# Kernel tuning notes

Measured on AMD Instinct MI355X. Metric: run time of the kernel, lower is better.

## Reference

```python
import jax, jax.numpy as jnp
import numpy as np

B, N, DIM_S, E = 128, 2048, 128, 128


def _xavier(key, shape):
    fan_out, fan_in = shape[0], shape[1]
    limit = float(np.sqrt(6.0 / (fan_in + fan_out)))
    return jax.random.uniform(key, shape, jnp.float32, -limit, limit)


def setup_inputs() -> dict:
    key = jax.random.key(0)
    ks = jax.random.split(key, 14)
    return {
        "instance": jax.random.normal(ks[0], (B, N, DIM_S), jnp.float32),
        # conv1d kernel-size-1 embeds == per-node linear layers [out, in]
        "W_s": _xavier(ks[1], (E, DIM_S)),
        "b_s": jnp.zeros((E,), jnp.float32),
        "W_a": _xavier(ks[2], (E, E)),
        "b_a": jnp.zeros((E,), jnp.float32),
        "v_a": jax.random.normal(ks[3], (E,), jnp.float32),
        "W_c": _xavier(ks[4], (E, 2 * E)),
        "b_c": jnp.zeros((E,), jnp.float32),
        "v_c": jax.random.normal(ks[5], (E,), jnp.float32),
        "W1": _xavier(ks[6], (E, E)),
        "b1": jnp.zeros((E,), jnp.float32),
        "W2": _xavier(ks[7], (1, E)),
        "b2": jnp.zeros((1,), jnp.float32),
    }


def reference(instance, W_s, b_s, W_a, b_a, v_a, W_c, b_c, v_c, W1, b1, W2, b2):
    # project_s: conv1d k=1 == linear over feature dim. [B,N,E]
    proj = jnp.einsum("bns,es->bne", instance, W_s) + b_s
    # first additive-attention score: v_a . tanh(w_a(proj))  -> [B,N]
    u_t = jnp.einsum("bne,e->bn", jnp.tanh(jnp.einsum("bne,fe->bnf", proj, W_a) + b_a), v_a)
    a_t = jax.nn.softmax(u_t, axis=1)  # softmax over nodes
    c_t = a_t[:, :, None] * proj  # [B,N,E]
    hidden_2 = jnp.concatenate([proj, c_t], axis=2)  # [B,N,2E]
    u_t_2 = jnp.einsum("bne,e->bn", jnp.tanh(jnp.einsum("bnf,ef->bne", hidden_2, W_c) + b_c), v_c)
    prob = jax.nn.softmax(u_t_2, axis=1)  # [B,N]
    h_i = jnp.einsum("bn,bne->be", prob, proj)  # weighted sum -> [B,E]
    out1 = jax.nn.relu(h_i @ W1.T + b1)  # [B,E]
    v = (out1 @ W2.T + b2)[:, 0]  # [B]
    return v
```

## Files before the change

### kernel.cpp

```cpp
#include <hip/hip_runtime.h>
#include <hip/hip_bf16.h>

typedef _Float16 half8 __attribute__((ext_vector_type(8)));
typedef _Float16 half4v __attribute__((ext_vector_type(4)));
typedef float f32x4 __attribute__((ext_vector_type(4)));

#define SWZ(byte, r) ((unsigned)(byte) ^ ((((unsigned)(r)) & 7u) << 4))

constexpr int Bb = 128;
constexpr int Nn = 2048;
constexpr int Ee = 128;
constexpr int BM = 64;
constexpr int NBLK = (Bb * Nn) / BM;

constexpr size_t OFF_W    = 0;
constexpr size_t OFF_PROJ = 131072;
constexpr size_t OFF_UT   = OFF_PROJ + (size_t)Bb * Nn * Ee * 2;
constexpr size_t OFF_AT   = OFF_UT   + (size_t)Bb * Nn * 4;
constexpr size_t OFF_UT2  = OFF_AT   + (size_t)Bb * Nn * 4;
constexpr size_t OFF_PROB = OFF_UT2  + (size_t)Bb * Nn * 4;
constexpr size_t OFF_HP   = OFF_PROB + (size_t)Bb * Nn * 4;

__device__ __forceinline__ void cp16(void* lds, const void* g) {
    __builtin_amdgcn_global_load_lds(
        (const __attribute__((address_space(1))) unsigned int*)g,
        (__attribute__((address_space(3))) unsigned int*)lds, 16, 0, 0);
}

__device__ __forceinline__ float fast_tanh(float x) {
    float e = __expf(2.0f * x);
    return 1.0f - 2.0f * __builtin_amdgcn_rcpf(e + 1.0f);
}

__global__ __launch_bounds__(256) void k_prep(const float* __restrict__ Ws,
                                              const float* __restrict__ Wa,
                                              const float* __restrict__ Wc,
                                              char* __restrict__ wdst)
{
    int id = blockIdx.x * 256 + threadIdx.x;
    for (int i = id; i < 65536; i += 64 * 256) {
        int mat = i >> 14;
        int rem = i & 16383;
        int r = rem >> 7, c = rem & 127;
        float v;
        if      (mat == 0) v = Ws[r * 128 + c];
        else if (mat == 1) v = Wa[r * 128 + c];
        else if (mat == 2) v = Wc[r * 256 + c];
        else               v = Wc[r * 256 + 128 + c];
        unsigned off = SWZ((unsigned)((r * 128 + c) * 2), r);
        *reinterpret_cast<_Float16*>(wdst + (size_t)mat * 32768 + off) = (_Float16)v;
    }
}

__global__ __launch_bounds__(256) void k_pass1(const float* __restrict__ inst,
                                               const char* __restrict__ wtiles,
                                               const float* __restrict__ bs,
                                               const float* __restrict__ ba,
                                               const float* __restrict__ va,
                                               char* __restrict__ projg,
                                               float* __restrict__ ut)
{
    __shared__ _Float16 ldsA[BM * 128];
    __shared__ _Float16 ldsW[128 * 128];

    const int tid  = threadIdx.x;
    const int lane = tid & 63;
    const int w    = tid >> 6;
    const int l15  = lane & 15;
    const int kg   = lane >> 4;
    const size_t row0 = (size_t)blockIdx.x * BM;

    float4 v[8];
    {
        const float* src = inst + row0 * 128;
        #pragma unroll
        for (int i = 0; i < 8; ++i)
            v[i] = *reinterpret_cast<const float4*>(src + (size_t)(i * 256 + tid) * 4);
    }
    #pragma unroll
    for (int i = 0; i < 8; ++i) {
        unsigned o = (unsigned)((i * 256 + tid) * 16);
        cp16((char*)ldsW + o, wtiles + o);
    }
    #pragma unroll
    for (int i = 0; i < 8; ++i) {
        int f = i * 256 + tid;
        int r = f >> 5, c4 = f & 31;
        half4v h = { (_Float16)v[i].x, (_Float16)v[i].y, (_Float16)v[i].z, (_Float16)v[i].w };
        unsigned off = SWZ((unsigned)(r * 256 + c4 * 8), r);
        *reinterpret_cast<half4v*>((char*)ldsA + off) = h;
    }
    __syncthreads();

    const int arow = w * 16 + l15;

    f32x4 acc[8];
    #pragma unroll
    for (int fr = 0; fr < 8; ++fr) acc[fr] = f32x4{0.f, 0.f, 0.f, 0.f};
    #pragma unroll
    for (int kk = 0; kk < 4; ++kk) {
        unsigned aoff = SWZ((unsigned)(arow * 256 + kk * 64 + kg * 16), arow);
        half8 af = *reinterpret_cast<const half8*>((char*)ldsA + aoff);
        #pragma unroll
        for (int fr = 0; fr < 8; ++fr) {
            int br = fr * 16 + l15;
            unsigned boff = SWZ((unsigned)(br * 256 + kk * 64 + kg * 16), br);
            half8 bf = *reinterpret_cast<const half8*>((char*)ldsW + boff);
            acc[fr] = __builtin_amdgcn_mfma_f32_16x16x32_f16(af, bf, acc[fr], 0, 0, 0);
        }
    }
    __syncthreads();

    #pragma unroll
    for (int i = 0; i < 8; ++i) {
        unsigned o = (unsigned)((i * 256 + tid) * 16);
        cp16((char*)ldsW + o, wtiles + 32768 + o);
    }
    #pragma unroll
    for (int fr = 0; fr < 8; ++fr) {
        int e = fr * 16 + l15;
        float bsv = bs[e];
        #pragma unroll
        for (int j = 0; j < 4; ++j) {
            int r = w * 16 + kg * 4 + j;
            float pv = acc[fr][j] + bsv;
            unsigned off = SWZ((unsigned)(r * 256 + e * 2), r);
            *reinterpret_cast<_Float16*>((char*)ldsA + off) = (_Float16)pv;
        }
    }
    __syncthreads();

    {
        char* dst = projg + row0 * 256;
        #pragma unroll
        for (int i = 0; i < 4; ++i) {
            unsigned o = (unsigned)((i * 256 + tid) * 16);
            *reinterpret_cast<uint4*>(dst + o) =
                *reinterpret_cast<const uint4*>((const char*)ldsA + o);
        }
    }

    f32x4 tac[8];
    #pragma unroll
    for (int fr = 0; fr < 8; ++fr) tac[fr] = f32x4{0.f, 0.f, 0.f, 0.f};
    #pragma unroll
    for (int kk = 0; kk < 4; ++kk) {
        unsigned aoff = SWZ((unsigned)(arow * 256 + kk * 64 + kg * 16), arow);
        half8 af = *reinterpret_cast<const half8*>((char*)ldsA + aoff);
        #pragma unroll
        for (int fr = 0; fr < 8; ++fr) {
            int br = fr * 16 + l15;
            unsigned boff = SWZ((unsigned)(br * 256 + kk * 64 + kg * 16), br);
            half8 bf = *reinterpret_cast<const half8*>((char*)ldsW + boff);
            tac[fr] = __builtin_amdgcn_mfma_f32_16x16x32_f16(af, bf, tac[fr], 0, 0, 0);
        }
    }
    float u[4] = {0.f, 0.f, 0.f, 0.f};
    #pragma unroll
    for (int fr = 0; fr < 8; ++fr) {
        int fcol = fr * 16 + l15;
        float vav = va[fcol], bav = ba[fcol];
        #pragma unroll
        for (int j = 0; j < 4; ++j)
            u[j] += vav * fast_tanh(tac[fr][j] + bav);
    }
    #pragma unroll
    for (int d = 1; d < 16; d <<= 1) {
        #pragma unroll
        for (int j = 0; j < 4; ++j) u[j] += __shfl_xor(u[j], d);
    }
    if (l15 == 0) {
        #pragma unroll
        for (int j = 0; j < 4; ++j)
            ut[row0 + w * 16 + kg * 4 + j] = u[j];
    }
}

__global__ __launch_bounds__(256) void k_softmax(const float* __restrict__ x,
                                                 float* __restrict__ y)
{
    __shared__ float red[4];
    const int b = blockIdx.x, tid = threadIdx.x;
    const int lane = tid & 63, w = tid >> 6;
    const float* xb = x + (size_t)b * Nn;
    float4 v0 = *reinterpret_cast<const float4*>(xb + tid * 8);
    float4 v1 = *reinterpret_cast<const float4*>(xb + tid * 8 + 4);
    float m = fmaxf(fmaxf(fmaxf(v0.x, v0.y), fmaxf(v0.z, v0.w)),
                    fmaxf(fmaxf(v1.x, v1.y), fmaxf(v1.z, v1.w)));
    #pragma unroll
    for (int d = 1; d < 64; d <<= 1) m = fmaxf(m, __shfl_xor(m, d));
    if (lane == 0) red[w] = m;
    __syncthreads();
    float M = fmaxf(fmaxf(red[0], red[1]), fmaxf(red[2], red[3]));
    float e[8] = { __expf(v0.x - M), __expf(v0.y - M), __expf(v0.z - M), __expf(v0.w - M),
                   __expf(v1.x - M), __expf(v1.y - M), __expf(v1.z - M), __expf(v1.w - M) };
    float s = 0.f;
    #pragma unroll
    for (int i = 0; i < 8; ++i) s += e[i];
    #pragma unroll
    for (int d = 1; d < 64; d <<= 1) s += __shfl_xor(s, d);
    __syncthreads();
    if (lane == 0) red[w] = s;
    __syncthreads();
    float inv = 1.0f / (red[0] + red[1] + red[2] + red[3]);
    float* yb = y + (size_t)b * Nn;
    float4 o0 = { e[0] * inv, e[1] * inv, e[2] * inv, e[3] * inv };
    float4 o1 = { e[4] * inv, e[5] * inv, e[6] * inv, e[7] * inv };
    *reinterpret_cast<float4*>(yb + tid * 8)     = o0;
    *reinterpret_cast<float4*>(yb + tid * 8 + 4) = o1;
}

__global__ __launch_bounds__(256) void k_pass2(const char* __restrict__ projg,
                                               const char* __restrict__ wtiles,
                                               const float* __restrict__ bc,
                                               const float* __restrict__ vc,
                                               const float* __restrict__ at,
                                               float* __restrict__ ut2)
{
    __shared__ _Float16 ldsP [BM * 128];
    __shared__ _Float16 ldsW1[128 * 128];
    __shared__ _Float16 ldsW2[128 * 128];

    const int tid  = threadIdx.x;
    const int lane = tid & 63;
    const int w    = tid >> 6;
    const int l15  = lane & 15;
    const int kg   = lane >> 4;
    const size_t row0 = (size_t)blockIdx.x * BM;

    {
        const char* src = projg + row0 * 256;
        #pragma unroll
        for (int i = 0; i < 4; ++i) {
            unsigned o = (unsigned)((i * 256 + tid) * 16);
            cp16((char*)ldsP + o, src + o);
        }
    }
    #pragma unroll
    for (int i = 0; i < 8; ++i) {
        unsigned o = (unsigned)((i * 256 + tid) * 16);
        cp16((char*)ldsW1 + o, wtiles + 65536 + o);
    }
    #pragma unroll
    for (int i = 0; i < 8; ++i) {
        unsigned o = (unsigned)((i * 256 + tid) * 16);
        cp16((char*)ldsW2 + o, wtiles + 98304 + o);
    }
    float aj[4];
    #pragma unroll
    for (int j = 0; j < 4; ++j) aj[j] = at[row0 + w * 16 + kg * 4 + j];
    __syncthreads();

    const int arow = w * 16 + l15;
    f32x4 u1[8], u2[8];
    #pragma unroll
    for (int fr = 0; fr < 8; ++fr) { u1[fr] = f32x4{0.f,0.f,0.f,0.f}; u2[fr] = f32x4{0.f,0.f,0.f,0.f}; }
    #pragma unroll
    for (int kk = 0; kk < 4; ++kk) {
        unsigned aoff = SWZ((unsigned)(arow * 256 + kk * 64 + kg * 16), arow);
        half8 af = *reinterpret_cast<const half8*>((char*)ldsP + aoff);
        #pragma unroll
        for (int fr = 0; fr < 8; ++fr) {
            int br = fr * 16 + l15;
            unsigned boff = SWZ((unsigned)(br * 256 + kk * 64 + kg * 16), br);
            half8 bf1 = *reinterpret_cast<const half8*>((char*)ldsW1 + boff);
            u1[fr] = __builtin_amdgcn_mfma_f32_16x16x32_f16(af, bf1, u1[fr], 0, 0, 0);
            half8 bf2 = *reinterpret_cast<const half8*>((char*)ldsW2 + boff);
            u2[fr] = __builtin_amdgcn_mfma_f32_16x16x32_f16(af, bf2, u2[fr], 0, 0, 0);
        }
    }

    float u[4] = {0.f, 0.f, 0.f, 0.f};
    #pragma unroll
    for (int fr = 0; fr < 8; ++fr) {
        int fcol = fr * 16 + l15;
        float vcv = vc[fcol], bcv = bc[fcol];
        #pragma unroll
        for (int j = 0; j < 4; ++j)
            u[j] += vcv * fast_tanh(u1[fr][j] + aj[j] * u2[fr][j] + bcv);
    }
    #pragma unroll
    for (int d = 1; d < 16; d <<= 1) {
        #pragma unroll
        for (int j = 0; j < 4; ++j) u[j] += __shfl_xor(u[j], d);
    }
    if (l15 == 0) {
        #pragma unroll
        for (int j = 0; j < 4; ++j)
            ut2[row0 + w * 16 + kg * 4 + j] = u[j];
    }
}

__global__ __launch_bounds__(256) void k_hi(const float* __restrict__ prob,
                                            const char* __restrict__ projg,
                                            float* __restrict__ hpart)
{
    __shared__ float pw[128];
    __shared__ float hp[16][128];

    const int bid = blockIdx.x;
    const int b = bid >> 4, chunk = bid & 15;
    const int n0 = chunk * 128;
    const int tid = threadIdx.x;
    const int rg = tid >> 4, c16 = tid & 15;

    if (tid < 128) pw[tid] = prob[(size_t)b * Nn + n0 + tid];
    __syncthreads();

    const char* pb = projg + ((size_t)b * Nn + n0) * 256;
    float acc[8] = {0.f,0.f,0.f,0.f,0.f,0.f,0.f,0.f};
    #pragma unroll
    for (int it = 0; it < 8; ++it) {
        int nl = rg + it * 16;
        float wgt = pw[nl];
        unsigned off = (unsigned)(nl * 256 + ((c16 * 16) ^ ((nl & 7) << 4)));
        half8 ph = *reinterpret_cast<const half8*>(pb + off);
        #pragma unroll
        for (int j = 0; j < 8; ++j) acc[j] += wgt * (float)ph[j];
    }
    #pragma unroll
    for (int j = 0; j < 8; ++j) hp[rg][c16 * 8 + j] = acc[j];
    __syncthreads();
    if (tid < 128) {
        float s = 0.f;
        #pragma unroll
        for (int k = 0; k < 16; ++k) s += hp[k][tid];
        hpart[((size_t)b * 16 + chunk) * 128 + tid] = s;
    }
}

__global__ __launch_bounds__(128) void k_head(const float* __restrict__ hpart,
                                              const float* __restrict__ W1,
                                              const float* __restrict__ b1,
                                              const float* __restrict__ W2,
                                              const float* __restrict__ b2,
                                              float* __restrict__ out)
{
    __shared__ float h[128];
    __shared__ float o1[128];
    const int b = blockIdx.x, tid = threadIdx.x;

    float s = 0.f;
    #pragma unroll
    for (int c = 0; c < 16; ++c) s += hpart[((size_t)b * 16 + c) * 128 + tid];
    h[tid] = s;
    __syncthreads();

    const float* wr = W1 + tid * 128;
    float o = b1[tid];
    #pragma unroll 8
    for (int e = 0; e < 128; e += 4) {
        float4 wv = *reinterpret_cast<const float4*>(wr + e);
        o += wv.x * h[e] + wv.y * h[e+1] + wv.z * h[e+2] + wv.w * h[e+3];
    }
    o1[tid] = fmaxf(o, 0.f);
    __syncthreads();

    if (tid < 64) {
        float p = o1[tid] * W2[tid] + o1[tid + 64] * W2[tid + 64];
        #pragma unroll
        for (int d = 1; d < 64; d <<= 1) p += __shfl_xor(p, d);
        if (tid == 0) out[b] = p + b2[0];
    }
}

extern "C" void kernel_launch(void* const* d_in, const int* in_sizes, int n_in,
                              void* d_out, int out_size, void* d_ws, size_t ws_size,
                              hipStream_t stream)
{
    const float* inst = (const float*)d_in[0];
    const float* Ws   = (const float*)d_in[1];
    const float* bs   = (const float*)d_in[2];
    const float* Wa   = (const float*)d_in[3];
    const float* ba   = (const float*)d_in[4];
    const float* va   = (const float*)d_in[5];
    const float* Wc   = (const float*)d_in[6];
    const float* bc   = (const float*)d_in[7];
    const float* vc   = (const float*)d_in[8];
    const float* W1   = (const float*)d_in[9];
    const float* b1   = (const float*)d_in[10];
    const float* W2   = (const float*)d_in[11];
    const float* b2   = (const float*)d_in[12];
    float* out = (float*)d_out;

    char*  ws     = (char*)d_ws;
    char*  wtiles = ws + OFF_W;
    char*  projg  = ws + OFF_PROJ;
    float* ut     = (float*)(ws + OFF_UT);
    float* at     = (float*)(ws + OFF_AT);
    float* ut2    = (float*)(ws + OFF_UT2);
    float* prob   = (float*)(ws + OFF_PROB);
    float* hpart  = (float*)(ws + OFF_HP);

    hipLaunchKernelGGL(k_prep,    dim3(64),   dim3(256), 0, stream, Ws, Wa, Wc, wtiles);
    hipLaunchKernelGGL(k_pass1,   dim3(NBLK), dim3(256), 0, stream, inst, wtiles, bs, ba, va, projg, ut);
    hipLaunchKernelGGL(k_softmax, dim3(Bb),   dim3(256), 0, stream, ut, at);
    hipLaunchKernelGGL(k_pass2,   dim3(NBLK), dim3(256), 0, stream, projg, wtiles, bc, vc, at, ut2);
    hipLaunchKernelGGL(k_softmax, dim3(Bb),   dim3(256), 0, stream, ut2, prob);
    hipLaunchKernelGGL(k_hi,      dim3(Bb*16),dim3(256), 0, stream, prob, projg, hpart);
    hipLaunchKernelGGL(k_head,    dim3(Bb),   dim3(128), 0, stream, hpart, W1, b1, W2, b2, out);
}
```

Baseline: 284.8 us.

## Make attention passes persistent with double-buffered LDS and fuse softmaxes

```diff
diff --git a/kernel.cpp b/kernel.cpp
--- a/kernel.cpp
+++ b/kernel.cpp
@@ -10,16 +10,15 @@
 constexpr int Bb = 128;
 constexpr int Nn = 2048;
 constexpr int Ee = 128;
-constexpr int BM = 64;
-constexpr int NBLK = (Bb * Nn) / BM;
+constexpr int BM1 = 128;
+constexpr int P1_BLOCKS = 256;
+constexpr int P1_ITERS = (Bb * Nn) / BM1 / P1_BLOCKS;
 
 constexpr size_t OFF_W    = 0;
 constexpr size_t OFF_PROJ = 131072;
 constexpr size_t OFF_UT   = OFF_PROJ + (size_t)Bb * Nn * Ee * 2;
-constexpr size_t OFF_AT   = OFF_UT   + (size_t)Bb * Nn * 4;
-constexpr size_t OFF_UT2  = OFF_AT   + (size_t)Bb * Nn * 4;
-constexpr size_t OFF_PROB = OFF_UT2  + (size_t)Bb * Nn * 4;
-constexpr size_t OFF_HP   = OFF_PROB + (size_t)Bb * Nn * 4;
+constexpr size_t OFF_UT2  = OFF_UT   + (size_t)Bb * Nn * 4;
+constexpr size_t OFF_HP   = OFF_UT2  + (size_t)Bb * Nn * 4;
 
 __device__ __forceinline__ void cp16(void* lds, const void* g) {
     __builtin_amdgcn_global_load_lds(
@@ -52,7 +51,7 @@
     }
 }
 
-__global__ __launch_bounds__(256) void k_pass1(const float* __restrict__ inst,
+__global__ __launch_bounds__(512) void k_pass1(const float* __restrict__ inst,
                                                const char* __restrict__ wtiles,
                                                const float* __restrict__ bs,
                                                const float* __restrict__ ba,
@@ -60,258 +59,301 @@
                                                char* __restrict__ projg,
                                                float* __restrict__ ut)
 {
-    __shared__ _Float16 ldsA[BM * 128];
-    __shared__ _Float16 ldsW[128 * 128];
+    __shared__ _Float16 ldsW[2 * 16384];
+    __shared__ _Float16 bufA[2][16384];
 
     const int tid  = threadIdx.x;
     const int lane = tid & 63;
     const int w    = tid >> 6;
     const int l15  = lane & 15;
     const int kg   = lane >> 4;
-    const size_t row0 = (size_t)blockIdx.x * BM;
-
+    const int arow = w * 16 + l15;
+
+    #pragma unroll
+    for (int i = 0; i < 8; ++i) {
+        unsigned o = (unsigned)((i * 512 + tid) * 16);
+        cp16((char*)ldsW + o, wtiles + o);
+    }
+
+    const size_t tile0 = (size_t)blockIdx.x * P1_ITERS;
     float4 v[8];
     {
-        const float* src = inst + row0 * 128;
+        const float* src = inst + tile0 * BM1 * 128;
         #pragma unroll
         for (int i = 0; i < 8; ++i)
-            v[i] = *reinterpret_cast<const float4*>(src + (size_t)(i * 256 + tid) * 4);
+            v[i] = *reinterpret_cast<const float4*>(src + (size_t)(i * 512 + tid) * 4);
     }
     #pragma unroll
     for (int i = 0; i < 8; ++i) {
-        unsigned o = (unsigned)((i * 256 + tid) * 16);
-        cp16((char*)ldsW + o, wtiles + o);
-    }
-    #pragma unroll
-    for (int i = 0; i < 8; ++i) {
-        int f = i * 256 + tid;
+        int f = i * 512 + tid;
         int r = f >> 5, c4 = f & 31;
         half4v h = { (_Float16)v[i].x, (_Float16)v[i].y, (_Float16)v[i].z, (_Float16)v[i].w };
-        unsigned off = SWZ((unsigned)(r * 256 + c4 * 8), r);
-        *reinterpret_cast<half4v*>((char*)ldsA + off) = h;
-    }
-    __syncthreads();
-
-    const int arow = w * 16 + l15;
-
-    f32x4 acc[8];
-    #pragma unroll
-    for (int fr = 0; fr < 8; ++fr) acc[fr] = f32x4{0.f, 0.f, 0.f, 0.f};
-    #pragma unroll
-    for (int kk = 0; kk < 4; ++kk) {
-        unsigned aoff = SWZ((unsigned)(arow * 256 + kk * 64 + kg * 16), arow);
-        half8 af = *reinterpret_cast<const half8*>((char*)ldsA + aoff);
+        *reinterpret_cast<half4v*>((char*)bufA[0] + SWZ(r * 256 + c4 * 8, r)) = h;
+    }
+    __syncthreads();
+
+    for (int it = 0; it < P1_ITERS; ++it) {
+        const int cur = it & 1, nxt = cur ^ 1;
+        const size_t row0 = (tile0 + it) * BM1;
+
+        if (it + 1 < P1_ITERS) {
+            const float* src = inst + (row0 + BM1) * 128;
+            #pragma unroll
+            for (int i = 0; i < 8; ++i)
+                v[i] = *reinterpret_cast<const float4*>(src + (size_t)(i * 512 + tid) * 4);
+        }
+
+        f32x4 acc[8];
+        #pragma unroll
+        for (int fr = 0; fr < 8; ++fr) acc[fr] = f32x4{0.f, 0.f, 0.f, 0.f};
+        #pragma unroll
+        for (int kk = 0; kk < 4; ++kk) {
+            half8 af = *reinterpret_cast<const half8*>(
+                (char*)bufA[cur] + SWZ(arow * 256 + kk * 64 + kg * 16, arow));
+            #pragma unroll
+            for (int fr = 0; fr < 8; ++fr) {
+                int br = fr * 16 + l15;
+                half8 bf = *reinterpret_cast<const half8*>(
+                    (char*)ldsW + SWZ(br * 256 + kk * 64 + kg * 16, br));
+                acc[fr] = __builtin_amdgcn_mfma_f32_16x16x32_f16(af, bf, acc[fr], 0, 0, 0);
+            }
+        }
+        __syncthreads();
+
         #pragma unroll
         for (int fr = 0; fr < 8; ++fr) {
-            int br = fr * 16 + l15;
-            unsigned boff = SWZ((unsigned)(br * 256 + kk * 64 + kg * 16), br);
-            half8 bf = *reinterpret_cast<const half8*>((char*)ldsW + boff);
-            acc[fr] = __builtin_amdgcn_mfma_f32_16x16x32_f16(af, bf, acc[fr], 0, 0, 0);
-        }
-    }
-    __syncthreads();
-
-    #pragma unroll
-    for (int i = 0; i < 8; ++i) {
-        unsigned o = (unsigned)((i * 256 + tid) * 16);
-        cp16((char*)ldsW + o, wtiles + 32768 + o);
-    }
-    #pragma unroll
-    for (int fr = 0; fr < 8; ++fr) {
-        int e = fr * 16 + l15;
-        float bsv = bs[e];
-        #pragma unroll
-        for (int j = 0; j < 4; ++j) {
-            int r = w * 16 + kg * 4 + j;
-            float pv = acc[fr][j] + bsv;
-            unsigned off = SWZ((unsigned)(r * 256 + e * 2), r);
-            *reinterpret_cast<_Float16*>((char*)ldsA + off) = (_Float16)pv;
-        }
-    }
-    __syncthreads();
-
-    {
-        char* dst = projg + row0 * 256;
-        #pragma unroll
-        for (int i = 0; i < 4; ++i) {
-            unsigned o = (unsigned)((i * 256 + tid) * 16);
-            *reinterpret_cast<uint4*>(dst + o) =
-                *reinterpret_cast<const uint4*>((const char*)ldsA + o);
-        }
-    }
-
-    f32x4 tac[8];
-    #pragma unroll
-    for (int fr = 0; fr < 8; ++fr) tac[fr] = f32x4{0.f, 0.f, 0.f, 0.f};
-    #pragma unroll
-    for (int kk = 0; kk < 4; ++kk) {
-        unsigned aoff = SWZ((unsigned)(arow * 256 + kk * 64 + kg * 16), arow);
-        half8 af = *reinterpret_cast<const half8*>((char*)ldsA + aoff);
+            int e = fr * 16 + l15;
+            float bsv = bs[e];
+            #pragma unroll
+            for (int j = 0; j < 4; ++j) {
+                int r = w * 16 + kg * 4 + j;
+                *reinterpret_cast<_Float16*>((char*)bufA[cur] + SWZ(r * 256 + e * 2, r)) =
+                    (_Float16)(acc[fr][j] + bsv);
+            }
+        }
+        if (it + 1 < P1_ITERS) {
+            #pragma unroll
+            for (int i = 0; i < 8; ++i) {
+                int f = i * 512 + tid;
+                int r = f >> 5, c4 = f & 31;
+                half4v h = { (_Float16)v[i].x, (_Float16)v[i].y, (_Float16)v[i].z, (_Float16)v[i].w };
+                *reinterpret_cast<half4v*>((char*)bufA[nxt] + SWZ(r * 256 + c4 * 8, r)) = h;
+            }
+        }
+        __syncthreads();
+
+        f32x4 tac[8];
+        #pragma unroll
+        for (int fr = 0; fr < 8; ++fr) tac[fr] = f32x4{0.f, 0.f, 0.f, 0.f};
+        #pragma unroll
+        for (int kk = 0; kk < 4; ++kk) {
+            half8 af = *reinterpret_cast<const half8*>(
+                (char*)bufA[cur] + SWZ(arow * 256 + kk * 64 + kg * 16, arow));
+            #pragma unroll
+            for (int fr = 0; fr < 8; ++fr) {
+                int br = fr * 16 + l15;
+                half8 bf = *reinterpret_cast<const half8*>(
+                    (char*)ldsW + 32768 + SWZ(br * 256 + kk * 64 + kg * 16, br));
+                tac[fr] = __builtin_amdgcn_mfma_f32_16x16x32_f16(af, bf, tac[fr], 0, 0, 0);
+            }
+        }
+
+        {
+            char* dst = projg + row0 * 256;
+            #pragma unroll
+            for (int i = 0; i < 4; ++i) {
+                unsigned o = (unsigned)((i * 512 + tid) * 16);
+                *reinterpret_cast<uint4*>(dst + o) =
+                    *reinterpret_cast<const uint4*>((const char*)bufA[cur] + o);
+            }
+        }
+
+        float u[4] = {0.f, 0.f, 0.f, 0.f};
         #pragma unroll
         for (int fr = 0; fr < 8; ++fr) {
-            int br = fr * 16 + l15;
-            unsigned boff = SWZ((unsigned)(br * 256 + kk * 64 + kg * 16), br);
-            half8 bf = *reinterpret_cast<const half8*>((char*)ldsW + boff);
-            tac[fr] = __builtin_amdgcn_mfma_f32_16x16x32_f16(af, bf, tac[fr], 0, 0, 0);
-        }
-    }
-    float u[4] = {0.f, 0.f, 0.f, 0.f};
-    #pragma unroll
-    for (int fr = 0; fr < 8; ++fr) {
-        int fcol = fr * 16 + l15;
-        float vav = va[fcol], bav = ba[fcol];
-        #pragma unroll
-        for (int j = 0; j < 4; ++j)
-            u[j] += vav * fast_tanh(tac[fr][j] + bav);
-    }
-    #pragma unroll
-    for (int d = 1; d < 16; d <<= 1) {
-        #pragma unroll
-        for (int j = 0; j < 4; ++j) u[j] += __shfl_xor(u[j], d);
-    }
-    if (l15 == 0) {
-        #pragma unroll
-        for (int j = 0; j < 4; ++j)
-            ut[row0 + w * 16 + kg * 4 + j] = u[j];
-    }
-}
-
-__global__ __launch_bounds__(256) void k_softmax(const float* __restrict__ x,
-                                                 float* __restrict__ y)
-{
-    __shared__ float red[4];
-    const int b = blockIdx.x, tid = threadIdx.x;
-    const int lane = tid & 63, w = tid >> 6;
-    const float* xb = x + (size_t)b * Nn;
-    float4 v0 = *reinterpret_cast<const float4*>(xb + tid * 8);
-    float4 v1 = *reinterpret_cast<const float4*>(xb + tid * 8 + 4);
-    float m = fmaxf(fmaxf(fmaxf(v0.x, v0.y), fmaxf(v0.z, v0.w)),
-                    fmaxf(fmaxf(v1.x, v1.y), fmaxf(v1.z, v1.w)));
-    #pragma unroll
-    for (int d = 1; d < 64; d <<= 1) m = fmaxf(m, __shfl_xor(m, d));
-    if (lane == 0) red[w] = m;
-    __syncthreads();
-    float M = fmaxf(fmaxf(red[0], red[1]), fmaxf(red[2], red[3]));
-    float e[8] = { __expf(v0.x - M), __expf(v0.y - M), __expf(v0.z - M), __expf(v0.w - M),
-                   __expf(v1.x - M), __expf(v1.y - M), __expf(v1.z - M), __expf(v1.w - M) };
-    float s = 0.f;
-    #pragma unroll
-    for (int i = 0; i < 8; ++i) s += e[i];
-    #pragma unroll
-    for (int d = 1; d < 64; d <<= 1) s += __shfl_xor(s, d);
-    __syncthreads();
-    if (lane == 0) red[w] = s;
-    __syncthreads();
-    float inv = 1.0f / (red[0] + red[1] + red[2] + red[3]);
-    float* yb = y + (size_t)b * Nn;
-    float4 o0 = { e[0] * inv, e[1] * inv, e[2] * inv, e[3] * inv };
-    float4 o1 = { e[4] * inv, e[5] * inv, e[6] * inv, e[7] * inv };
-    *reinterpret_cast<float4*>(yb + tid * 8)     = o0;
-    *reinterpret_cast<float4*>(yb + tid * 8 + 4) = o1;
-}
-
-__global__ __launch_bounds__(256) void k_pass2(const char* __restrict__ projg,
+            int fcol = fr * 16 + l15;
+            float vav = va[fcol], bav = ba[fcol];
+            #pragma unroll
+            for (int j = 0; j < 4; ++j)
+                u[j] += vav * fast_tanh(tac[fr][j] + bav);
+        }
+        #pragma unroll
+        for (int d = 1; d < 16; d <<= 1) {
+            #pragma unroll
+            for (int j = 0; j < 4; ++j) u[j] += __shfl_xor(u[j], d);
+        }
+        if (l15 == 0) {
+            #pragma unroll
+            for (int j = 0; j < 4; ++j)
+                ut[row0 + w * 16 + kg * 4 + j] = u[j];
+        }
+    }
+}
+
+__global__ __launch_bounds__(512) void k_pass2(const char* __restrict__ projg,
                                                const char* __restrict__ wtiles,
                                                const float* __restrict__ bc,
                                                const float* __restrict__ vc,
-                                               const float* __restrict__ at,
+                                               const float* __restrict__ ut,
                                                float* __restrict__ ut2)
 {
-    __shared__ _Float16 ldsP [BM * 128];
-    __shared__ _Float16 ldsW1[128 * 128];
-    __shared__ _Float16 ldsW2[128 * 128];
+    __shared__ _Float16 ldsW[2 * 16384];
+    __shared__ _Float16 bufP[2][16384];
+    __shared__ float at_lds[1024];
+    __shared__ float redm[8], reds[8];
 
     const int tid  = threadIdx.x;
     const int lane = tid & 63;
     const int w    = tid >> 6;
     const int l15  = lane & 15;
     const int kg   = lane >> 4;
-    const size_t row0 = (size_t)blockIdx.x * BM;
-
-    {
-        const char* src = projg + row0 * 256;
-        #pragma unroll
-        for (int i = 0; i < 4; ++i) {
-            unsigned o = (unsigned)((i * 256 + tid) * 16);
-            cp16((char*)ldsP + o, src + o);
-        }
-    }
+    const int arow = w * 16 + l15;
+    const int bid  = blockIdx.x;
+    const int batch = bid >> 1, half = bid & 1;
+
+    const float* utb = ut + (size_t)batch * Nn;
+    float4 x = *reinterpret_cast<const float4*>(utb + tid * 4);
+    float m = fmaxf(fmaxf(x.x, x.y), fmaxf(x.z, x.w));
+    #pragma unroll
+    for (int d = 1; d < 64; d <<= 1) m = fmaxf(m, __shfl_xor(m, d));
+    if (lane == 0) redm[w] = m;
+    __syncthreads();
+    float M = redm[0];
+    #pragma unroll
+    for (int k = 1; k < 8; ++k) M = fmaxf(M, redm[k]);
+    float e0 = __expf(x.x - M), e1 = __expf(x.y - M), e2 = __expf(x.z - M), e3 = __expf(x.w - M);
+    float s = e0 + e1 + e2 + e3;
+    #pragma unroll
+    for (int d = 1; d < 64; d <<= 1) s += __shfl_xor(s, d);
+    if (lane == 0) reds[w] = s;
+    __syncthreads();
+    float S = 0.f;
+    #pragma unroll
+    for (int k = 0; k < 8; ++k) S += reds[k];
+    float invS = 1.0f / S;
+
     #pragma unroll
     for (int i = 0; i < 8; ++i) {
-        unsigned o = (unsigned)((i * 256 + tid) * 16);
-        cp16((char*)ldsW1 + o, wtiles + 65536 + o);
-    }
-    #pragma unroll
-    for (int i = 0; i < 8; ++i) {
-        unsigned o = (unsigned)((i * 256 + tid) * 16);
-        cp16((char*)ldsW2 + o, wtiles + 98304 + o);
-    }
-    float aj[4];
-    #pragma unroll
-    for (int j = 0; j < 4; ++j) aj[j] = at[row0 + w * 16 + kg * 4 + j];
-    __syncthreads();
-
-    const int arow = w * 16 + l15;
-    f32x4 u1[8], u2[8];
-    #pragma unroll
-    for (int fr = 0; fr < 8; ++fr) { u1[fr] = f32x4{0.f,0.f,0.f,0.f}; u2[fr] = f32x4{0.f,0.f,0.f,0.f}; }
-    #pragma unroll
-    for (int kk = 0; kk < 4; ++kk) {
-        unsigned aoff = SWZ((unsigned)(arow * 256 + kk * 64 + kg * 16), arow);
-        half8 af = *reinterpret_cast<const half8*>((char*)ldsP + aoff);
+        unsigned o = (unsigned)((i * 512 + tid) * 16);
+        cp16((char*)ldsW + o, wtiles + 65536 + o);
+    }
+    const char* psrc = projg + ((size_t)batch * Nn + (size_t)half * 1024) * 256;
+    #pragma unroll
+    for (int i = 0; i < 4; ++i) {
+        unsigned o = (unsigned)((i * 512 + tid) * 16);
+        cp16((char*)bufP[0] + o, psrc + o);
+    }
+    if ((tid >> 8) == half) {
+        int rl = (tid & 255) * 4;
+        at_lds[rl + 0] = e0 * invS;
+        at_lds[rl + 1] = e1 * invS;
+        at_lds[rl + 2] = e2 * invS;
+        at_lds[rl + 3] = e3 * invS;
+    }
+
+    for (int it = 0; it < 8; ++it) {
+        const int cur = it & 1, nxt = cur ^ 1;
+        __syncthreads();
+
+        if (it + 1 < 8) {
+            #pragma unroll
+            for (int i = 0; i < 4; ++i) {
+                unsigned o = (unsigned)((i * 512 + tid) * 16);
+                cp16((char*)bufP[nxt] + o, psrc + (size_t)(it + 1) * 32768 + o);
+            }
+        }
+
+        f32x4 u1[8], u2[8];
+        #pragma unroll
+        for (int fr = 0; fr < 8; ++fr) { u1[fr] = f32x4{0.f,0.f,0.f,0.f}; u2[fr] = f32x4{0.f,0.f,0.f,0.f}; }
+        #pragma unroll
+        for (int kk = 0; kk < 4; ++kk) {
+            half8 af = *reinterpret_cast<const half8*>(
+                (char*)bufP[cur] + SWZ(arow * 256 + kk * 64 + kg * 16, arow));
+            #pragma unroll
+            for (int fr = 0; fr < 8; ++fr) {
+                int br = fr * 16 + l15;
+                half8 bf1 = *reinterpret_cast<const half8*>(
+                    (char*)ldsW + SWZ(br * 256 + kk * 64 + kg * 16, br));
+                u1[fr] = __builtin_amdgcn_mfma_f32_16x16x32_f16(af, bf1, u1[fr], 0, 0, 0);
+                half8 bf2 = *reinterpret_cast<const half8*>(
+                    (char*)ldsW + 32768 + SWZ(br * 256 + kk * 64 + kg * 16, br));
+                u2[fr] = __builtin_amdgcn_mfma_f32_16x16x32_f16(af, bf2, u2[fr], 0, 0, 0);
+            }
+        }
+
+        float aj[4];
+        #pragma unroll
+        for (int j = 0; j < 4; ++j) aj[j] = at_lds[it * 128 + w * 16 + kg * 4 + j];
+        float u[4] = {0.f, 0.f, 0.f, 0.f};
         #pragma unroll
         for (int fr = 0; fr < 8; ++fr) {
-            int br = fr * 16 + l15;
-            unsigned boff = SWZ((unsigned)(br * 256 + kk * 64 + kg * 16), br);
-            half8 bf1 = *reinterpret_cast<const half8*>((char*)ldsW1 + boff);
-            u1[fr] = __builtin_amdgcn_mfma_f32_16x16x32_f16(af, bf1, u1[fr], 0, 0, 0);
-            half8 bf2 = *reinterpret_cast<const half8*>((char*)ldsW2 + boff);
-            u2[fr] = __builtin_amdgcn_mfma_f32_16x16x32_f16(af, bf2, u2[fr], 0, 0, 0);
-        }
-    }
-
-    float u[4] = {0.f, 0.f, 0.f, 0.f};
-    #pragma unroll
-    for (int fr = 0; fr < 8; ++fr) {
-        int fcol = fr * 16 + l15;
-        float vcv = vc[fcol], bcv = bc[fcol];
-        #pragma unroll
-        for (int j = 0; j < 4; ++j)
-            u[j] += vcv * fast_tanh(u1[fr][j] + aj[j] * u2[fr][j] + bcv);
-    }
-    #pragma unroll
-    for (int d = 1; d < 16; d <<= 1) {
-        #pragma unroll
-        for (int j = 0; j < 4; ++j) u[j] += __shfl_xor(u[j], d);
-    }
-    if (l15 == 0) {
-        #pragma unroll
-        for (int j = 0; j < 4; ++j)
-            ut2[row0 + w * 16 + kg * 4 + j] = u[j];
-    }
-}
-
-__global__ __launch_bounds__(256) void k_hi(const float* __restrict__ prob,
+            int fcol = fr * 16 + l15;
+            float vcv = vc[fcol], bcv = bc[fcol];
+            #pragma unroll
+            for (int j = 0; j < 4; ++j)
+                u[j] += vcv * fast_tanh(u1[fr][j] + aj[j] * u2[fr][j] + bcv);
+        }
+        #pragma unroll
+        for (int d = 1; d < 16; d <<= 1) {
+            #pragma unroll
+            for (int j = 0; j < 4; ++j) u[j] += __shfl_xor(u[j], d);
+        }
+        if (l15 == 0) {
+            #pragma unroll
+            for (int j = 0; j < 4; ++j)
+                ut2[(size_t)batch * Nn + (size_t)half * 1024 + it * 128 + w * 16 + kg * 4 + j] = u[j];
+        }
+    }
+}
+
+__global__ __launch_bounds__(256) void k_hi(const float* __restrict__ ut2,
                                             const char* __restrict__ projg,
                                             float* __restrict__ hpart)
 {
     __shared__ float pw[128];
     __shared__ float hp[16][128];
+    __shared__ float redm[4], reds[4];
 
     const int bid = blockIdx.x;
     const int b = bid >> 4, chunk = bid & 15;
     const int n0 = chunk * 128;
     const int tid = threadIdx.x;
+    const int lane = tid & 63, w = tid >> 6;
+
+    const float* u2b = ut2 + (size_t)b * Nn;
+    float4 x0 = *reinterpret_cast<const float4*>(u2b + tid * 8);
+    float4 x1 = *reinterpret_cast<const float4*>(u2b + tid * 8 + 4);
+    float m = fmaxf(fmaxf(fmaxf(x0.x, x0.y), fmaxf(x0.z, x0.w)),
+                    fmaxf(fmaxf(x1.x, x1.y), fmaxf(x1.z, x1.w)));
+    #pragma unroll
+    for (int d = 1; d < 64; d <<= 1) m = fmaxf(m, __shfl_xor(m, d));
+    if (lane == 0) redm[w] = m;
+    __syncthreads();
+    float M = fmaxf(fmaxf(redm[0], redm[1]), fmaxf(redm[2], redm[3]));
+    float e[8] = { __expf(x0.x - M), __expf(x0.y - M), __expf(x0.z - M), __expf(x0.w - M),
+                   __expf(x1.x - M), __expf(x1.y - M), __expf(x1.z - M), __expf(x1.w - M) };
+    float s = 0.f;
+    #pragma unroll
+    for (int i = 0; i < 8; ++i) s += e[i];
+    #pragma unroll
+    for (int d = 1; d < 64; d <<= 1) s += __shfl_xor(s, d);
+    if (lane == 0) reds[w] = s;
+    __syncthreads();
+    float inv = 1.0f / (reds[0] + reds[1] + reds[2] + reds[3]);
+    if ((tid >> 4) == chunk) {
+        int base = (tid & 15) * 8;
+        #pragma unroll
+        for (int k = 0; k < 8; ++k) pw[base + k] = e[k] * inv;
+    }
+    __syncthreads();
+
     const int rg = tid >> 4, c16 = tid & 15;
-
-    if (tid < 128) pw[tid] = prob[(size_t)b * Nn + n0 + tid];
-    __syncthreads();
-
     const char* pb = projg + ((size_t)b * Nn + n0) * 256;
     float acc[8] = {0.f,0.f,0.f,0.f,0.f,0.f,0.f,0.f};
     #pragma unroll
-    for (int it = 0; it < 8; ++it) {
-        int nl = rg + it * 16;
+    for (int itn = 0; itn < 8; ++itn) {
+        int nl = rg + itn * 16;
         float wgt = pw[nl];
         unsigned off = (unsigned)(nl * 256 + ((c16 * 16) ^ ((nl & 7) << 4)));
         half8 ph = *reinterpret_cast<const half8*>(pb + off);
@@ -322,10 +364,10 @@
     for (int j = 0; j < 8; ++j) hp[rg][c16 * 8 + j] = acc[j];
     __syncthreads();
     if (tid < 128) {
-        float s = 0.f;
-        #pragma unroll
-        for (int k = 0; k < 16; ++k) s += hp[k][tid];
-        hpart[((size_t)b * 16 + chunk) * 128 + tid] = s;
+        float s2 = 0.f;
+        #pragma unroll
+        for (int k = 0; k < 16; ++k) s2 += hp[k][tid];
+        hpart[((size_t)b * 16 + chunk) * 128 + tid] = s2;
     }
 }
 
@@ -387,16 +429,12 @@
     char*  wtiles = ws + OFF_W;
     char*  projg  = ws + OFF_PROJ;
     float* ut     = (float*)(ws + OFF_UT);
-    float* at     = (float*)(ws + OFF_AT);
     float* ut2    = (float*)(ws + OFF_UT2);
-    float* prob   = (float*)(ws + OFF_PROB);
     float* hpart  = (float*)(ws + OFF_HP);
 
-    hipLaunchKernelGGL(k_prep,    dim3(64),   dim3(256), 0, stream, Ws, Wa, Wc, wtiles);
-    hipLaunchKernelGGL(k_pass1,   dim3(NBLK), dim3(256), 0, stream, inst, wtiles, bs, ba, va, projg, ut);
-    hipLaunchKernelGGL(k_softmax, dim3(Bb),   dim3(256), 0, stream, ut, at);
-    hipLaunchKernelGGL(k_pass2,   dim3(NBLK), dim3(256), 0, stream, projg, wtiles, bc, vc, at, ut2);
-    hipLaunchKernelGGL(k_softmax, dim3(Bb),   dim3(256), 0, stream, ut2, prob);
-    hipLaunchKernelGGL(k_hi,      dim3(Bb*16),dim3(256), 0, stream, prob, projg, hpart);
-    hipLaunchKernelGGL(k_head,    dim3(Bb),   dim3(128), 0, stream, hpart, W1, b1, W2, b2, out);
-}
+    hipLaunchKernelGGL(k_prep,  dim3(64),        dim3(256), 0, stream, Ws, Wa, Wc, wtiles);
+    hipLaunchKernelGGL(k_pass1, dim3(P1_BLOCKS), dim3(512), 0, stream, inst, wtiles, bs, ba, va, projg, ut);
+    hipLaunchKernelGGL(k_pass2, dim3(Bb * 2),    dim3(512), 0, stream, projg, wtiles, bc, vc, ut, ut2);
+    hipLaunchKernelGGL(k_hi,    dim3(Bb * 16),   dim3(256), 0, stream, ut2, projg, hpart);
+    hipLaunchKernelGGL(k_head,  dim3(Bb),        dim3(128), 0, stream, hpart, W1, b1, W2, b2, out);
+}
```

New measurement: 285.1 us. About the same (+0.1%).
